# Kernel optimization log

Measured on AMD Instinct MI355X. Metric: run time of the kernel, lower is better.

## Reference

```python
import jax, jax.numpy as jnp
import numpy as np

N = 4096          # num nodes
D = 128           # feature dim (dataset.x.shape[-1])
E = 131072        # num edges (avg degree 32)
POOL_K = 0.6      # ks[0]
K = max(2, int(POOL_K * N))  # 2457 kept nodes


def setup_inputs() -> dict:
    key = jax.random.key(0)
    ks = jax.random.split(key, 8)
    s = 0.05
    g = jax.random.randint(ks[0], (2, E), 0, N)                      # edge_index
    h = jax.random.normal(ks[1], (N, D), jnp.float32)                # node features
    Wd = jax.random.normal(ks[2], (D, D), jnp.float32) * s           # down-GCN stub
    bd = jnp.zeros((D,), jnp.float32)
    pw = jax.random.normal(ks[3], (D, 1), jnp.float32) * s           # Pool.proj weight
    pb = jnp.zeros((1,), jnp.float32)                                # Pool.proj bias
    Wb = jax.random.normal(ks[4], (D, D), jnp.float32) * s           # bottom-GCN stub
    bb = jnp.zeros((D,), jnp.float32)
    Wu = jax.random.normal(ks[5], (D, D), jnp.float32) * s           # up-GCN stub
    bu = jnp.zeros((D,), jnp.float32)
    return {"g": g, "h": h, "Wd": Wd, "bd": bd, "pw": pw, "pb": pb,
            "Wb": Wb, "bb": bb, "Wu": Wu, "bu": bu}


def reference(g, h, Wd, bd, pw, pb, Wb, bb, Wu, bu):
    dt = h.dtype
    src, dst = g[0], g[1]
    # to_dense_adj: scatter-add edges into dense [N, N] adjacency
    adj = jnp.zeros((N, N), dt).at[src, dst].add(jnp.ones((E,), dt))

    # down GCN (GNNEarly stub, called with h only): linear
    h0 = h @ Wd + bd

    # Pool: score, topk, gather
    scores = jax.nn.sigmoid((h0 @ pw + pb)[:, 0])          # [N]
    values, idx = jax.lax.top_k(scores, K)                 # descending, like torch.topk
    new_h = h0[idx] * values[:, None]                      # [K, D]

    # boolean 2-hop connectivity, then subselect pooled nodes
    un_g = (adj > 0).astype(dt)
    two_hop = ((un_g @ un_g) > 0).astype(dt)               # [N, N]
    sub = two_hop[idx][:, idx]                             # [K, K]
    # norm_g: g / degrees with torch broadcasting => column-normalize by row-degree
    degrees = jnp.sum(sub, axis=1)                         # [K]
    g_p = sub / degrees                                    # sub[i,j] / degrees[j]

    # bottom GCN (stub with pooled graph): propagate + linear
    h_b = g_p @ (new_h @ Wb) + bb                          # [K, D]

    # Unpool: scatter back to N nodes
    h_u = jnp.zeros((N, D), dt).at[idx].set(h_b)

    # up GCN (stub with original dense adj adj_ms[0])
    h_up = adj @ (h_u @ Wu) + bu                           # [N, D]

    h1 = h_up + h0        # h.add(down_outs[0])
    h2 = h1 + h           # h.add(org_h)
    return (h1, h2)       # hs list
```

## Files before the change

kernel.cpp:

```cpp
#include <hip/hip_runtime.h>
#include <hip/hip_bf16.h>
#include <stdint.h>


#define NN 4096
#define DD 128
#define KKEEP 2457
#define SUBW 40
#define MP 2464
#define KP 2560
#define MT 154
#define NT 8
#define KCHUNK (KP / 4)
#define RT 8
#define TBLK 160

typedef unsigned long long u64;
typedef unsigned short ushort_t;
typedef __attribute__((ext_vector_type(8))) short bf16x8;
typedef __attribute__((ext_vector_type(4))) float f32x4;

__global__ void k_zero(float4* __restrict__ p) {
    int i = blockIdx.x * 256 + threadIdx.x;
    p[i] = make_float4(0.f, 0.f, 0.f, 0.f);
}

__global__ void k_h0_build(const float* __restrict__ h, const float* __restrict__ Wd,
                           const float* __restrict__ bd, const float* __restrict__ pw,
                           const float* __restrict__ pb, const int* __restrict__ g, int E,
                           const float* __restrict__ Wb, const float* __restrict__ Wu,
                           const float* __restrict__ bb,
                           float* __restrict__ h0, float* __restrict__ scores,
                           u64* __restrict__ rowbits, int* __restrict__ deg,
                           float* __restrict__ W2, float* __restrict__ cu) {
    __shared__ float rows[RT][DD];
    __shared__ float sred[2][RT];
    int bid = blockIdx.x;
    int d = threadIdx.x;
    if (bid >= 1536) {
        int wb = bid - 1536;
        if (wb < 16) {
            int r0 = wb * RT;
            #pragma unroll
            for (int r = 0; r < RT; ++r) rows[r][d] = Wb[(size_t)(r0 + r) * DD + d];
            __syncthreads();
            float acc[RT];
            #pragma unroll
            for (int r = 0; r < RT; ++r) acc[r] = 0.f;
            for (int kb = 0; kb < DD; kb += 16) {
                float w[16];
                #pragma unroll
                for (int j = 0; j < 16; ++j) w[j] = Wu[(size_t)(kb + j) * DD + d];
                #pragma unroll
                for (int r = 0; r < RT; ++r)
                    #pragma unroll
                    for (int j = 0; j < 16; ++j) acc[r] += rows[r][kb + j] * w[j];
            }
            #pragma unroll
            for (int r = 0; r < RT; ++r) W2[(size_t)(r0 + r) * DD + d] = acc[r];
        } else {
            float a = 0.f;
            for (int m = 0; m < DD; ++m) a += bb[m] * Wu[(size_t)m * DD + d];
            cu[d] = a;
        }
        return;
    }
    if (bid >= 512) {
        int e = (bid - 512) * 128 + d;
        if (e < E) {
            int s = g[e], d2 = g[E + e];
            atomicOr(&rowbits[(size_t)s * 64 + (d2 >> 6)], 1ull << (d2 & 63));
            atomicAdd(&deg[s], 1);
        }
        return;
    }
    int r0 = bid * RT;
    #pragma unroll
    for (int r = 0; r < RT; ++r) rows[r][d] = h[(size_t)(r0 + r) * DD + d];
    __syncthreads();
    float acc[RT];
    float b = bd[d];
    #pragma unroll
    for (int r = 0; r < RT; ++r) acc[r] = b;
    for (int kb = 0; kb < DD; kb += 16) {
        float w[16];
        #pragma unroll
        for (int j = 0; j < 16; ++j) w[j] = Wd[(size_t)(kb + j) * DD + d];
        #pragma unroll
        for (int r = 0; r < RT; ++r)
            #pragma unroll
            for (int j = 0; j < 16; ++j) acc[r] += rows[r][kb + j] * w[j];
    }
    #pragma unroll
    for (int r = 0; r < RT; ++r) h0[(size_t)(r0 + r) * DD + d] = acc[r];
    float pwd = pw[d];
    int lane = d & 63, wv = d >> 6;
    #pragma unroll
    for (int r = 0; r < RT; ++r) {
        float v = acc[r] * pwd;
        #pragma unroll
        for (int s = 32; s > 0; s >>= 1) v += __shfl_xor(v, s);
        if (lane == 0) sred[wv][r] = v;
    }
    __syncthreads();
    if (d < RT) {
        float v = sred[0][d] + sred[1][d];
        scores[r0 + d] = 1.0f / (1.0f + expf(-(v + pb[0])));
    }
}

__global__ void k_rank_scan(const float* __restrict__ scores, const int* __restrict__ deg,
                            int* __restrict__ keep, int* __restrict__ pos,
                            int* __restrict__ idxl, int* __restrict__ off) {
    int bid = blockIdx.x;
    int t = threadIdx.x;
    if (bid == NN / 4) {
        __shared__ int part[256];
        int base = t * 16;
        int loc[16]; int s = 0;
        #pragma unroll
        for (int i = 0; i < 16; ++i) { loc[i] = s; s += deg[base + i]; }
        part[t] = s;
        __syncthreads();
        int sum = 0;
        for (int i = 0; i < t; ++i) sum += part[i];
        #pragma unroll
        for (int i = 0; i < 16; ++i) off[base + i] = sum + loc[i];
        if (t == 255) off[NN] = sum + s;
        return;
    }
    int lane = t & 63;
    int i = bid * 4 + (t >> 6);
    float my = scores[i];
    int rank = 0;
    #pragma unroll 4
    for (int base = 0; base < NN; base += 64) {
        int jj = base + lane;
        float sj = scores[jj];
        u64 m = __ballot((sj > my) || (sj == my && jj < i));
        rank += __popcll(m);
    }
    if (lane == 0) {
        if (rank < KKEEP) { keep[i] = 1; pos[i] = rank; idxl[rank] = i; }
        else keep[i] = 0;
    }
}

__global__ void k_sub_scatter_t(const u64* __restrict__ rowbits, const int* __restrict__ idxl,
                                const int* __restrict__ g, int E, const int* __restrict__ off,
                                const int* __restrict__ keep, const int* __restrict__ pos,
                                int* __restrict__ cursor, int* __restrict__ csrv,
                                u64* __restrict__ subbits, ushort_t* __restrict__ invdegb,
                                const float* __restrict__ h0, const float* __restrict__ scores,
                                const float* __restrict__ W2, ushort_t* __restrict__ tT) {
    __shared__ float rowsLDS[16][DD];
    __shared__ int nb[320];
    __shared__ int nbcnt;
    __shared__ int cntS;
    __shared__ u64 accLDS[64];
    int bid = blockIdx.x;
    int t = threadIdx.x;
    if (bid >= MP + 512) {
        int u = bid - (MP + 512);
        int half = t >> 7, d = t & 127;
        int r0 = u * 16 + half * 8;
        float (*rows)[DD] = &rowsLDS[half * 8];
        #pragma unroll
        for (int r = 0; r < RT; ++r) {
            int rr = r0 + r;
            float v = 0.f;
            if (rr < KKEEP) {
                int i = idxl[rr];
                v = h0[(size_t)i * DD + d] * scores[i];
            }
            rows[r][d] = v;
        }
        __syncthreads();
        float acc[RT];
        #pragma unroll
        for (int r = 0; r < RT; ++r) acc[r] = 0.f;
        for (int kb = 0; kb < DD; kb += 16) {
            float w[16];
            #pragma unroll
            for (int j = 0; j < 16; ++j) w[j] = W2[(size_t)(kb + j) * DD + d];
            #pragma unroll
            for (int r = 0; r < RT; ++r)
                #pragma unroll
                for (int j = 0; j < 16; ++j) acc[r] += rows[r][kb + j] * w[j];
        }
        bf16x8 packed;
        #pragma unroll
        for (int r = 0; r < RT; ++r) {
            __hip_bfloat16 b = __float2bfloat16(acc[r]);
            packed[r] = *reinterpret_cast<short*>(&b);
        }
        *reinterpret_cast<bf16x8*>(tT + (size_t)d * KP + r0) = packed;
        return;
    }
    if (bid >= MP) {
        int e = (bid - MP) * 256 + t;
        if (e < E) {
            int s = g[e], dd = g[E + e];
            int p = atomicAdd(&cursor[s], 1);
            csrv[off[s] + p] = keep[dd] ? pos[dd] : -1;
        }
        return;
    }
    int r = bid;
    int wv = t >> 6, lane = t & 63;
    if (r >= KKEEP) {
        if (t < SUBW) subbits[(size_t)r * SUBW + t] = 0;
        return;
    }
    int i = idxl[r];
    if (wv == 0) {
        u64 rw = rowbits[(size_t)i * 64 + lane];
        int myc = __popcll(rw);
        int pre = myc;
        #pragma unroll
        for (int s2 = 1; s2 < 64; s2 <<= 1) {
            int tt = __shfl_up(pre, s2);
            if (lane >= s2) pre += tt;
        }
        pre -= myc;
        u64 w = rw; int j = 0;
        while (w) {
            int b = __builtin_ctzll(w);
            w &= w - 1;
            nb[pre + j] = lane * 64 + b; ++j;
        }
        if (lane == 63) nbcnt = pre + myc;
    } else if (wv == 1) {
        accLDS[lane] = 0;
    } else if (wv == 2 && lane == 0) {
        cntS = 0;
    }
    __syncthreads();
    int cnt_nb = nbcnt;
    u64 accw = 0;
    for (int j = wv; j < cnt_nb; j += 4)
        accw |= rowbits[(size_t)nb[j] * 64 + lane];
    atomicOr(&accLDS[lane], accw);
    __syncthreads();
    u64 accw_full = accLDS[lane];
    int cntp = 0;
    #pragma unroll
    for (int wjj = 0; wjj < 10; ++wjj) {
        int wj = wv * 10 + wjj;
        int c = wj * 64 + lane;
        int ci = (c < KKEEP) ? idxl[c] : 0;
        u64 w = __shfl(accw_full, ci >> 6);
        int bit = (c < KKEEP) ? (int)((w >> (ci & 63)) & 1ull) : 0;
        u64 word = __ballot(bit);
        cntp += __popcll(word);
        if (lane == 0) subbits[(size_t)r * SUBW + wj] = word;
    }
    if (lane == 0) atomicAdd(&cntS, cntp);
    __syncthreads();
    if (t == 0) {
        __hip_bfloat16 b = __float2bfloat16(1.0f / (float)cntS);
        invdegb[r] = *reinterpret_cast<ushort_t*>(&b);
    }
}

__global__ void k_gemm(const u64* __restrict__ subbits, const ushort_t* __restrict__ invdegb,
                       const short* __restrict__ tT, const float* __restrict__ cu,
                       float* __restrict__ uu) {
    __shared__ f32x4 red[4][64];
    __shared__ uint4 lut[256];
    int t = threadIdx.x;
    {
        uint32_t m0 = ((t & 1) ? 0xFFFFu : 0u) | ((t & 2) ? 0xFFFF0000u : 0u);
        uint32_t m1 = ((t & 4) ? 0xFFFFu : 0u) | ((t & 8) ? 0xFFFF0000u : 0u);
        uint32_t m2 = ((t & 16) ? 0xFFFFu : 0u) | ((t & 32) ? 0xFFFF0000u : 0u);
        uint32_t m3 = ((t & 64) ? 0xFFFFu : 0u) | ((t & 128) ? 0xFFFF0000u : 0u);
        lut[t] = make_uint4(m0, m1, m2, m3);
    }
    __syncthreads();
    int bid = blockIdx.x;
    int tile = (bid & 7) * (MT * NT / 8) + (bid >> 3);
    int wv = t >> 6, lane = t & 63;
    int rt = tile >> 3, ct = tile & 7;
    const u64* abits = subbits + (size_t)(rt * 16 + (lane & 15)) * SUBW;
    const short* brow = tT + (size_t)(ct * 16 + (lane & 15)) * KP + ((lane >> 4) * 8) + wv * KCHUNK;
    int kbase = wv * KCHUNK + ((lane >> 4) * 8);
    f32x4 acc = {0.f, 0.f, 0.f, 0.f};
    #pragma unroll 4
    for (int kk = 0; kk < KCHUNK; kk += 32) {
        int k = kbase + kk;
        u64 w = abits[k >> 6];
        int byte = (int)((w >> (k & 63)) & 0xFFull);
        uint4 msk = lut[byte];
        uint4 ivb = *(const uint4*)(invdegb + k);
        uint4 af = make_uint4(msk.x & ivb.x, msk.y & ivb.y, msk.z & ivb.z, msk.w & ivb.w);
        bf16x8 a = *reinterpret_cast<bf16x8*>(&af);
        bf16x8 b = *(const bf16x8*)(brow + kk);
        acc = __builtin_amdgcn_mfma_f32_16x16x32_bf16(a, b, acc, 0, 0, 0);
    }
    red[wv][lane] = acc;
    __syncthreads();
    if (wv == 0) {
        f32x4 s = red[0][lane] + red[1][lane] + red[2][lane] + red[3][lane];
        int col = ct * 16 + (lane & 15);
        float cuv = cu[col];
        int row0 = rt * 16 + ((lane >> 4) * 4);
        #pragma unroll
        for (int j = 0; j < 4; ++j) {
            int row = row0 + j;
            if (row < KKEEP) uu[(size_t)row * DD + col] = s[j] + cuv;
        }
    }
}

__global__ void k_agg(const int* __restrict__ off, const int* __restrict__ csrv,
                      const float* __restrict__ uu, const float* __restrict__ bu,
                      const float* __restrict__ h0, const float* __restrict__ h,
                      float* __restrict__ out) {
    int s = blockIdx.x, d = threadIdx.x;
    int b = off[s], e2 = off[s + 1];
    float acc = 0.f;
    int k = b;
    for (; k + 4 <= e2; k += 4) {
        int v0 = csrv[k], v1 = csrv[k + 1], v2 = csrv[k + 2], v3 = csrv[k + 3];
        float a0 = (v0 >= 0) ? uu[(size_t)v0 * DD + d] : 0.f;
        float a1 = (v1 >= 0) ? uu[(size_t)v1 * DD + d] : 0.f;
        float a2 = (v2 >= 0) ? uu[(size_t)v2 * DD + d] : 0.f;
        float a3 = (v3 >= 0) ? uu[(size_t)v3 * DD + d] : 0.f;
        acc += (a0 + a1) + (a2 + a3);
    }
    for (; k < e2; ++k) {
        int v = csrv[k];
        if (v >= 0) acc += uu[(size_t)v * DD + d];
    }
    size_t o = (size_t)s * DD + d;
    float a = acc + bu[d] + h0[o];
    out[o] = a;
    out[(size_t)NN * DD + o] = a + h[o];
}

extern "C" void kernel_launch(void* const* d_in, const int* in_sizes, int n_in,
                              void* d_out, int out_size, void* d_ws, size_t ws_size,
                              hipStream_t stream) {
    const int*   g  = (const int*)d_in[0];
    const float* h  = (const float*)d_in[1];
    const float* Wd = (const float*)d_in[2];
    const float* bd = (const float*)d_in[3];
    const float* pw = (const float*)d_in[4];
    const float* pb = (const float*)d_in[5];
    const float* Wb = (const float*)d_in[6];
    const float* bb = (const float*)d_in[7];
    const float* Wu = (const float*)d_in[8];
    const float* bu = (const float*)d_in[9];
    float* out = (float*)d_out;
    int E = in_sizes[0] / 2;

    char* ws = (char*)d_ws;
    u64*      subbits = (u64*)  (ws + 0);
    u64*      rowbits = (u64*)  (ws + (13u << 20));
    int*      deg     = (int*)  (ws + (15u << 20));
    int*      cursor  = (int*)  (ws + (15u << 20) + 16384);
    int*      off     = (int*)  (ws + (15u << 20) + 32768);
    float*    h0      = (float*)(ws + (16u << 20));
    ushort_t* tT      = (ushort_t*)(ws + (18u << 20));
    int*      csrv    = (int*)  (ws + (21u << 20));
    float*    uu      = (float*)(ws + (22u << 20));
    float*    scores  = (float*)(ws + (24u << 20));
    ushort_t* invdegb = (ushort_t*)(ws + (24u << 20) + 16384);
    int*      pos     = (int*)  (ws + (24u << 20) + 32768);
    int*      keep    = (int*)  (ws + (24u << 20) + 49152);
    int*      idxl    = (int*)  (ws + (24u << 20) + 65536);
    float*    W2      = (float*)(ws + (24u << 20) + 98304);
    float*    cu      = (float*)(ws + (24u << 20) + 98304 + 65536);

    k_zero<<<520, 256, 0, stream>>>((float4*)rowbits);
    k_h0_build<<<1553, 128, 0, stream>>>(h, Wd, bd, pw, pb, g, E, Wb, Wu, bb,
                                         h0, scores, rowbits, deg, W2, cu);
    k_rank_scan<<<NN / 4 + 1, 256, 0, stream>>>(scores, deg, keep, pos, idxl, off);
    k_sub_scatter_t<<<MP + 512 + TBLK, 256, 0, stream>>>(rowbits, idxl, g, E, off,
                                                         keep, pos, cursor, csrv,
                                                         subbits, invdegb, h0, scores, W2, tT);
    k_gemm<<<MT * NT, 256, 0, stream>>>(subbits, invdegb, (const short*)tT, cu, uu);
    k_agg<<<NN, DD, 0, stream>>>(off, csrv, uu, bu, h0, h, out);
}
```

Baseline: 110.2 us.

## Precompute scaled h0·W2 for all nodes in h0 kernel; gather rows later

```diff
diff --git a/kernel.cpp b/kernel.cpp
--- a/kernel.cpp
+++ b/kernel.cpp
@@ -13,58 +13,58 @@
 #define NT 8
 #define KCHUNK (KP / 4)
 #define RT 8
-#define TBLK 160
 
 typedef unsigned long long u64;
 typedef unsigned short ushort_t;
 typedef __attribute__((ext_vector_type(8))) short bf16x8;
 typedef __attribute__((ext_vector_type(4))) float f32x4;
 
-__global__ void k_zero(float4* __restrict__ p) {
-    int i = blockIdx.x * 256 + threadIdx.x;
-    p[i] = make_float4(0.f, 0.f, 0.f, 0.f);
+__global__ void k_zero_w2(float4* __restrict__ zbase, const float* __restrict__ Wb,
+                          const float* __restrict__ Wu, const float* __restrict__ bb,
+                          float* __restrict__ W2, float* __restrict__ cu) {
+    __shared__ float rows[RT][DD];
+    int bid = blockIdx.x, d = threadIdx.x;
+    if (bid < 1040) {
+        zbase[bid * 128 + d] = make_float4(0.f, 0.f, 0.f, 0.f);
+        return;
+    }
+    if (bid < 1056) {
+        int r0 = (bid - 1040) * RT;
+        #pragma unroll
+        for (int r = 0; r < RT; ++r) rows[r][d] = Wb[(size_t)(r0 + r) * DD + d];
+        __syncthreads();
+        float acc[RT];
+        #pragma unroll
+        for (int r = 0; r < RT; ++r) acc[r] = 0.f;
+        for (int kb = 0; kb < DD; kb += 16) {
+            float w[16];
+            #pragma unroll
+            for (int j = 0; j < 16; ++j) w[j] = Wu[(size_t)(kb + j) * DD + d];
+            #pragma unroll
+            for (int r = 0; r < RT; ++r)
+                #pragma unroll
+                for (int j = 0; j < 16; ++j) acc[r] += rows[r][kb + j] * w[j];
+        }
+        #pragma unroll
+        for (int r = 0; r < RT; ++r) W2[(size_t)(r0 + r) * DD + d] = acc[r];
+        return;
+    }
+    float a = 0.f;
+    for (int m = 0; m < DD; ++m) a += bb[m] * Wu[(size_t)m * DD + d];
+    cu[d] = a;
 }
 
 __global__ void k_h0_build(const float* __restrict__ h, const float* __restrict__ Wd,
                            const float* __restrict__ bd, const float* __restrict__ pw,
                            const float* __restrict__ pb, const int* __restrict__ g, int E,
-                           const float* __restrict__ Wb, const float* __restrict__ Wu,
-                           const float* __restrict__ bb,
+                           const float* __restrict__ W2,
                            float* __restrict__ h0, float* __restrict__ scores,
-                           u64* __restrict__ rowbits, int* __restrict__ deg,
-                           float* __restrict__ W2, float* __restrict__ cu) {
+                           float* __restrict__ tall,
+                           u64* __restrict__ rowbits, int* __restrict__ deg) {
     __shared__ float rows[RT][DD];
     __shared__ float sred[2][RT];
     int bid = blockIdx.x;
     int d = threadIdx.x;
-    if (bid >= 1536) {
-        int wb = bid - 1536;
-        if (wb < 16) {
-            int r0 = wb * RT;
-            #pragma unroll
-            for (int r = 0; r < RT; ++r) rows[r][d] = Wb[(size_t)(r0 + r) * DD + d];
-            __syncthreads();
-            float acc[RT];
-            #pragma unroll
-            for (int r = 0; r < RT; ++r) acc[r] = 0.f;
-            for (int kb = 0; kb < DD; kb += 16) {
-                float w[16];
-                #pragma unroll
-                for (int j = 0; j < 16; ++j) w[j] = Wu[(size_t)(kb + j) * DD + d];
-                #pragma unroll
-                for (int r = 0; r < RT; ++r)
-                    #pragma unroll
-                    for (int j = 0; j < 16; ++j) acc[r] += rows[r][kb + j] * w[j];
-            }
-            #pragma unroll
-            for (int r = 0; r < RT; ++r) W2[(size_t)(r0 + r) * DD + d] = acc[r];
-        } else {
-            float a = 0.f;
-            for (int m = 0; m < DD; ++m) a += bb[m] * Wu[(size_t)m * DD + d];
-            cu[d] = a;
-        }
-        return;
-    }
     if (bid >= 512) {
         int e = (bid - 512) * 128 + d;
         if (e < E) {
@@ -94,6 +94,7 @@
     #pragma unroll
     for (int r = 0; r < RT; ++r) h0[(size_t)(r0 + r) * DD + d] = acc[r];
     float pwd = pw[d];
+    float pb0 = pb[0];
     int lane = d & 63, wv = d >> 6;
     #pragma unroll
     for (int r = 0; r < RT; ++r) {
@@ -105,8 +106,29 @@
     __syncthreads();
     if (d < RT) {
         float v = sred[0][d] + sred[1][d];
-        scores[r0 + d] = 1.0f / (1.0f + expf(-(v + pb[0])));
-    }
+        scores[r0 + d] = 1.0f / (1.0f + expf(-(v + pb0)));
+    }
+    float sc[RT];
+    #pragma unroll
+    for (int r = 0; r < RT; ++r)
+        sc[r] = 1.0f / (1.0f + expf(-(sred[0][r] + sred[1][r] + pb0)));
+    #pragma unroll
+    for (int r = 0; r < RT; ++r) rows[r][d] = acc[r] * sc[r];
+    __syncthreads();
+    float acc2[RT];
+    #pragma unroll
+    for (int r = 0; r < RT; ++r) acc2[r] = 0.f;
+    for (int kb = 0; kb < DD; kb += 16) {
+        float w[16];
+        #pragma unroll
+        for (int j = 0; j < 16; ++j) w[j] = W2[(size_t)(kb + j) * DD + d];
+        #pragma unroll
+        for (int r = 0; r < RT; ++r)
+            #pragma unroll
+            for (int j = 0; j < 16; ++j) acc2[r] += rows[r][kb + j] * w[j];
+    }
+    #pragma unroll
+    for (int r = 0; r < RT; ++r) tall[(size_t)(r0 + r) * DD + d] = acc2[r];
 }
 
 __global__ void k_rank_scan(const float* __restrict__ scores, const int* __restrict__ deg,
@@ -146,14 +168,12 @@
     }
 }
 
-__global__ void k_sub_scatter_t(const u64* __restrict__ rowbits, const int* __restrict__ idxl,
+__global__ void k_sub_scatter_g(const u64* __restrict__ rowbits, const int* __restrict__ idxl,
                                 const int* __restrict__ g, int E, const int* __restrict__ off,
                                 const int* __restrict__ keep, const int* __restrict__ pos,
                                 int* __restrict__ cursor, int* __restrict__ csrv,
                                 u64* __restrict__ subbits, ushort_t* __restrict__ invdegb,
-                                const float* __restrict__ h0, const float* __restrict__ scores,
-                                const float* __restrict__ W2, ushort_t* __restrict__ tT) {
-    __shared__ float rowsLDS[16][DD];
+                                const float* __restrict__ tall, ushort_t* __restrict__ tT) {
     __shared__ int nb[320];
     __shared__ int nbcnt;
     __shared__ int cntS;
@@ -163,38 +183,17 @@
     if (bid >= MP + 512) {
         int u = bid - (MP + 512);
         int half = t >> 7, d = t & 127;
-        int r0 = u * 16 + half * 8;
-        float (*rows)[DD] = &rowsLDS[half * 8];
-        #pragma unroll
-        for (int r = 0; r < RT; ++r) {
-            int rr = r0 + r;
+        int c0 = u * 16 + half * 8;
+        bf16x8 packed;
+        #pragma unroll
+        for (int r = 0; r < 8; ++r) {
+            int cc = c0 + r;
             float v = 0.f;
-            if (rr < KKEEP) {
-                int i = idxl[rr];
-                v = h0[(size_t)i * DD + d] * scores[i];
-            }
-            rows[r][d] = v;
-        }
-        __syncthreads();
-        float acc[RT];
-        #pragma unroll
-        for (int r = 0; r < RT; ++r) acc[r] = 0.f;
-        for (int kb = 0; kb < DD; kb += 16) {
-            float w[16];
-            #pragma unroll
-            for (int j = 0; j < 16; ++j) w[j] = W2[(size_t)(kb + j) * DD + d];
-            #pragma unroll
-            for (int r = 0; r < RT; ++r)
-                #pragma unroll
-                for (int j = 0; j < 16; ++j) acc[r] += rows[r][kb + j] * w[j];
-        }
-        bf16x8 packed;
-        #pragma unroll
-        for (int r = 0; r < RT; ++r) {
-            __hip_bfloat16 b = __float2bfloat16(acc[r]);
+            if (cc < KKEEP) v = tall[(size_t)idxl[cc] * DD + d];
+            __hip_bfloat16 b = __float2bfloat16(v);
             packed[r] = *reinterpret_cast<short*>(&b);
         }
-        *reinterpret_cast<bf16x8*>(tT + (size_t)d * KP + r0) = packed;
+        *reinterpret_cast<bf16x8*>(tT + (size_t)d * KP + c0) = packed;
         return;
     }
     if (bid >= MP) {
@@ -371,14 +370,15 @@
     int*      idxl    = (int*)  (ws + (24u << 20) + 65536);
     float*    W2      = (float*)(ws + (24u << 20) + 98304);
     float*    cu      = (float*)(ws + (24u << 20) + 98304 + 65536);
-
-    k_zero<<<520, 256, 0, stream>>>((float4*)rowbits);
-    k_h0_build<<<1553, 128, 0, stream>>>(h, Wd, bd, pw, pb, g, E, Wb, Wu, bb,
-                                         h0, scores, rowbits, deg, W2, cu);
+    float*    tall    = (float*)(ws + (26u << 20));
+
+    k_zero_w2<<<1057, 128, 0, stream>>>((float4*)rowbits, Wb, Wu, bb, W2, cu);
+    k_h0_build<<<1536, 128, 0, stream>>>(h, Wd, bd, pw, pb, g, E, W2,
+                                         h0, scores, tall, rowbits, deg);
     k_rank_scan<<<NN / 4 + 1, 256, 0, stream>>>(scores, deg, keep, pos, idxl, off);
-    k_sub_scatter_t<<<MP + 512 + TBLK, 256, 0, stream>>>(rowbits, idxl, g, E, off,
-                                                         keep, pos, cursor, csrv,
-                                                         subbits, invdegb, h0, scores, W2, tT);
+    k_sub_scatter_g<<<MP + 512 + 160, 256, 0, stream>>>(rowbits, idxl, g, E, off,
+                                                        keep, pos, cursor, csrv,
+                                                        subbits, invdegb, tall, tT);
     k_gemm<<<MT * NT, 256, 0, stream>>>(subbits, invdegb, (const short*)tT, cu, uu);
     k_agg<<<NN, DD, 0, stream>>>(off, csrv, uu, bu, h0, h, out);
 }
```

Result: slower. 118.8 us (+7.8%).
